# Kernel tuning notes

Hardware: AMD Instinct MI355X
Metric: run time of the kernel (lower is better)

## Reference

```python
import jax, jax.numpy as jnp
import numpy as np

A_BITS = 3
W_BITS = 3

def setup_inputs() -> dict:
    key = jax.random.key(0)
    k1, k2 = jax.random.split(key)
    # activations: small nonnegative ints (will be clipped to [0, 2^A_bits-1])
    x = jax.random.randint(k1, (32, 256, 56, 56), 0, 2 ** A_BITS, dtype=jnp.int32)
    # weights: torch.randint(0, 2**W_bits - 1, ...) -> values in [0, 6]
    weight = jax.random.randint(k2, (256, 256, 3, 3), 0, 2 ** W_BITS - 1).astype(jnp.float32)
    return {"x": x, "weight": weight}

def reference(x, weight):
    # quantize: clip activations to [0, 2^A_bits - 1]; truncate weight to int
    xq = jnp.clip(x.astype(jnp.int32), 0, 2 ** A_BITS - 1).astype(jnp.float32)
    wq = weight.astype(jnp.int32).astype(jnp.float32)  # OIHW, nonneg small ints
    # direct conv2d, stride 1, no padding (VALID). Small ints -> exact in fp32.
    out = jax.lax.conv_general_dilated(
        xq, wq,
        window_strides=(1, 1),
        padding="VALID",
        dimension_numbers=("NCHW", "OIHW", "NCHW"),
    )
    return out  # [32, 256, 54, 54]
```

## Files before the change

### kernel.cpp

```cpp
#include <hip/hip_runtime.h>
#include <stdint.h>

typedef int i32x4 __attribute__((ext_vector_type(4)));

#define N_IMG 32
#define C_IN 256
#define H_IN 56
#define W_IN 56
#define K_OUT 256
#define H_OUT 54
#define W_OUT 54
#define HW_OUT 2916
#define M_PIX 93312
#define CHW_OUT 746496

#define XT_BYTES ((size_t)N_IMG * H_IN * W_IN * C_IN)
#define WT_BYTES ((size_t)9 * K_OUT * C_IN)

__global__ __launch_bounds__(256) void xform_x(const int* __restrict__ x,
                                               unsigned char* __restrict__ xt) {
    const int bid = blockIdx.x;
    const int n = bid / H_IN;
    const int h = bid % H_IN;
    const int c = threadIdx.x;
    const int* src = x + ((size_t)((n * C_IN + c) * H_IN + h)) * W_IN;
    unsigned char* dst = xt + ((size_t)(n * H_IN + h) * W_IN) * C_IN + c;
    #pragma unroll
    for (int w0 = 0; w0 < W_IN; w0 += 4) {
        int4 v = *(const int4*)(src + w0);
        int a[4] = {v.x, v.y, v.z, v.w};
        #pragma unroll
        for (int j = 0; j < 4; ++j) {
            int q = a[j] < 0 ? 0 : (a[j] > 7 ? 7 : a[j]);
            dst[(size_t)(w0 + j) * C_IN] = (unsigned char)q;
        }
    }
}

__global__ __launch_bounds__(256) void xform_w(const float* __restrict__ w,
                                               unsigned char* __restrict__ wt) {
    const int k = blockIdx.x;
    const int c = threadIdx.x;
    const float* src = w + ((size_t)k * C_IN + c) * 9;
    #pragma unroll
    for (int rs = 0; rs < 9; ++rs) {
        int iv = (int)src[rs];
        wt[((size_t)rs * K_OUT + k) * C_IN + c] = (unsigned char)iv;
    }
}

__device__ __forceinline__ void gload_lds16(const void* g, void* l) {
    __builtin_amdgcn_global_load_lds(
        (const __attribute__((address_space(1))) uint32_t*)g,
        (__attribute__((address_space(3))) uint32_t*)l,
        16, 0, 0);
}

__global__ __launch_bounds__(256) void conv_mfma(const unsigned char* __restrict__ xt,
                                                 const unsigned char* __restrict__ wt,
                                                 float* __restrict__ out) {
    __shared__ unsigned char As[128 * 128];
    __shared__ unsigned char Bs[128 * 128];

    const int t   = threadIdx.x;
    const int l   = t & 63;
    const int wid = t >> 6;
    const int wr  = wid >> 1;
    const int wc  = wid & 1;
    const int mb  = blockIdx.x >> 1;
    const int nb  = blockIdx.x & 1;

    const int cs = (((l & 7) ^ (l >> 3)) << 4);

    int abase[4], bbase[4];
    #pragma unroll
    for (int i = 0; i < 4; ++i) {
        const int row = i * 32 + wid * 8 + (l >> 3);
        const int m   = mb * 128 + row;
        const int n   = m / HW_OUT;
        const int rem = m - n * HW_OUT;
        const int ho  = rem / W_OUT;
        const int wo  = rem - ho * W_OUT;
        abase[i] = (((n * H_IN + ho) * W_IN + wo) << 8) + cs;
        bbase[i] = ((nb * 128 + row) << 8) + cs;
    }

    i32x4 acc[4][4];
    #pragma unroll
    for (int i = 0; i < 4; ++i)
        #pragma unroll
        for (int j = 0; j < 4; ++j)
            acc[i][j] = (i32x4){0, 0, 0, 0};

    const char* xb = (const char*)xt;
    const char* wb = (const char*)wt;
    char* Ab = (char*)As;
    char* Bb = (char*)Bs;

    const int lrow = l & 15;
    const int lk   = (l >> 4) << 4;

    for (int ks = 0; ks < 18; ++ks) {
        const int rs  = ks >> 1;
        const int c0b = (ks & 1) << 7;
        const int r   = rs / 3;
        const int s   = rs - r * 3;
        const int astep = ((r * W_IN + s) << 8) + c0b;
        const int bstep = rs * (K_OUT * C_IN) + c0b;

        __syncthreads();
        #pragma unroll
        for (int i = 0; i < 4; ++i) {
            gload_lds16(xb + abase[i] + astep, Ab + i * 4096 + wid * 1024);
            gload_lds16(wb + bbase[i] + bstep, Bb + i * 4096 + wid * 1024);
        }
        __syncthreads();

        i32x4 af[4][2], bfv[4][2];
        #pragma unroll
        for (int f = 0; f < 4; ++f) {
            const int arow = wr * 64 + f * 16 + lrow;
            const int brow = wc * 64 + f * 16 + lrow;
            const int asw = (arow & 7) << 4;
            const int bsw = (brow & 7) << 4;
            #pragma unroll
            for (int kk = 0; kk < 2; ++kk) {
                const int chb = (kk << 6) + lk;
                af[f][kk]  = *(const i32x4*)(Ab + (arow << 7) + (chb ^ asw));
                bfv[f][kk] = *(const i32x4*)(Bb + (brow << 7) + (chb ^ bsw));
            }
        }
        #pragma unroll
        for (int mf = 0; mf < 4; ++mf)
            #pragma unroll
            for (int nf = 0; nf < 4; ++nf)
                #pragma unroll
                for (int kk = 0; kk < 2; ++kk)
                    acc[mf][nf] = __builtin_amdgcn_mfma_i32_16x16x64_i8(
                        af[mf][kk], bfv[nf][kk], acc[mf][nf], 0, 0, 0);
    }

    const int c16    = l & 15;
    const int p4     = (l >> 4) << 2;
    const int chbase = nb * 128 + wc * 64 + c16;
    #pragma unroll
    for (int mf = 0; mf < 4; ++mf) {
        #pragma unroll
        for (int j = 0; j < 4; ++j) {
            const int m   = mb * 128 + wr * 64 + mf * 16 + p4 + j;
            const int n   = m / HW_OUT;
            const int rem = m - n * HW_OUT;
            float* obase = out + (size_t)n * CHW_OUT + rem;
            #pragma unroll
            for (int nf = 0; nf < 4; ++nf)
                obase[(size_t)(chbase + nf * 16) * HW_OUT] = (float)acc[mf][nf][j];
        }
    }
}

__global__ __launch_bounds__(256) void conv_naive(const int* __restrict__ x,
                                                  const float* __restrict__ w,
                                                  float* __restrict__ out) {
    int idx = blockIdx.x * 256 + threadIdx.x;
    if (idx >= N_IMG * K_OUT * HW_OUT) return;
    const int wo = idx % W_OUT;
    int tmp = idx / W_OUT;
    const int ho = tmp % H_OUT; tmp /= H_OUT;
    const int k = tmp % K_OUT;
    const int n = tmp / K_OUT;
    float acc = 0.f;
    for (int c = 0; c < C_IN; ++c) {
        const int* xp = x + ((size_t)((n * C_IN + c) * H_IN + ho)) * W_IN + wo;
        const float* wp = w + ((size_t)(k * C_IN + c)) * 9;
        #pragma unroll
        for (int r = 0; r < 3; ++r)
            #pragma unroll
            for (int s = 0; s < 3; ++s) {
                int xv = xp[r * W_IN + s];
                xv = xv < 0 ? 0 : (xv > 7 ? 7 : xv);
                acc += (float)xv * (float)(int)wp[r * 3 + s];
            }
    }
    out[idx] = acc;
}

extern "C" void kernel_launch(void* const* d_in, const int* in_sizes, int n_in,
                              void* d_out, int out_size, void* d_ws, size_t ws_size,
                              hipStream_t stream) {
    const int*   x = (const int*)d_in[0];
    const float* w = (const float*)d_in[1];
    float* out = (float*)d_out;

    const size_t need = XT_BYTES + WT_BYTES;
    if (ws_size >= need) {
        unsigned char* xt = (unsigned char*)d_ws;
        unsigned char* wt = (unsigned char*)((char*)d_ws + XT_BYTES);
        hipLaunchKernelGGL(xform_x, dim3(N_IMG * H_IN), dim3(256), 0, stream, x, xt);
        hipLaunchKernelGGL(xform_w, dim3(K_OUT), dim3(256), 0, stream, w, wt);
        hipLaunchKernelGGL(conv_mfma, dim3((M_PIX / 128) * 2), dim3(256), 0, stream, xt, wt, out);
    } else {
        const int total = N_IMG * K_OUT * HW_OUT;
        hipLaunchKernelGGL(conv_naive, dim3((total + 255) / 256), dim3(256), 0, stream, x, w, out);
    }
}
```

Before: 102.6 us.

## Triple-buffer conv MFMA main loop with 512-thread 128x256 tiles

Reworks the int8 MFMA implicit-GEMM conv kernel. Each block now covers all 256 output channels with 8 waves (128x256 tile) instead of two blocks of 128x128, and a 3-stage LDS ring with global_load_lds prefetch two k-steps ahead is interleaved with split MFMA phases, using explicit barriers, waitcnt and setprio. The aim is to overlap global loads with MFMA work and halve the redundant activation loads. It uses 144KB of LDS per block and hand-tuned synchronisation, which risks low occupancy and subtle ordering bugs.

```diff
diff --git a/kernel.cpp b/kernel.cpp
--- a/kernel.cpp
+++ b/kernel.cpp
@@ -56,34 +56,131 @@
         16, 0, 0);
 }
 
-__global__ __launch_bounds__(256) void conv_mfma(const unsigned char* __restrict__ xt,
-                                                 const unsigned char* __restrict__ wt,
-                                                 float* __restrict__ out) {
-    __shared__ unsigned char As[128 * 128];
-    __shared__ unsigned char Bs[128 * 128];
-
-    const int t   = threadIdx.x;
-    const int l   = t & 63;
-    const int wid = t >> 6;
-    const int wr  = wid >> 1;
-    const int wc  = wid & 1;
-    const int mb  = blockIdx.x >> 1;
-    const int nb  = blockIdx.x & 1;
-
-    const int cs = (((l & 7) ^ (l >> 3)) << 4);
-
-    int abase[4], bbase[4];
-    #pragma unroll
-    for (int i = 0; i < 4; ++i) {
-        const int row = i * 32 + wid * 8 + (l >> 3);
-        const int m   = mb * 128 + row;
+__device__ __forceinline__ unsigned lds_off(const void* p) {
+    return (unsigned)(unsigned long long)(__attribute__((address_space(3))) const char*)p;
+}
+
+#define DSREAD(dst, addr) \
+    asm volatile("ds_read_b128 %0, %1" : "=v"(dst) : "v"(addr))
+#define WAIT_LGKM0 asm volatile("s_waitcnt lgkmcnt(0)" ::: "memory")
+
+template <bool PRE, int VM>
+__device__ __forceinline__ void kstep(int T, unsigned CA, unsigned CB,
+                                      unsigned char* PA, unsigned char* PB,
+                                      const char* xb, const char* wb,
+                                      const int* abase, const int* bbase,
+                                      const unsigned (&aoff)[4][2],
+                                      const unsigned (&boff)[4][2],
+                                      int tb16, i32x4 (&acc)[4][4]) {
+    int astp = 0, bstp = 0;
+    if constexpr (PRE) {
+        const int tp = T + 2;
+        const int rp = tp >> 1, cp = (tp & 1) << 7;
+        const int rr = rp / 3, ss = rp - rr * 3;
+        astp = ((rr * W_IN + ss) << 8) + cp;
+        bstp = rp * (K_OUT * C_IN) + cp;
+    }
+    i32x4 af[4][2], bf[4][2];
+    #pragma unroll
+    for (int mf = 0; mf < 4; ++mf)
+        #pragma unroll
+        for (int kk = 0; kk < 2; ++kk)
+            DSREAD(af[mf][kk], CA + aoff[mf][kk]);
+    #pragma unroll
+    for (int nf = 0; nf < 2; ++nf)
+        #pragma unroll
+        for (int kk = 0; kk < 2; ++kk)
+            DSREAD(bf[nf][kk], CB + boff[nf][kk]);
+    if constexpr (PRE) {
+        gload_lds16(xb + abase[0] + astp, PA + tb16);
+        gload_lds16(xb + abase[1] + astp, PA + 8192 + tb16);
+        gload_lds16(wb + bbase[0] + bstp, PB + tb16);
+    }
+    __builtin_amdgcn_s_barrier();
+    WAIT_LGKM0;
+    __builtin_amdgcn_sched_barrier(0);
+    __builtin_amdgcn_s_setprio(1);
+    #pragma unroll
+    for (int mf = 0; mf < 4; ++mf)
+        #pragma unroll
+        for (int nf = 0; nf < 2; ++nf)
+            #pragma unroll
+            for (int kk = 0; kk < 2; ++kk)
+                acc[mf][nf] = __builtin_amdgcn_mfma_i32_16x16x64_i8(
+                    af[mf][kk], bf[nf][kk], acc[mf][nf], 0, 0, 0);
+    __builtin_amdgcn_s_setprio(0);
+    __builtin_amdgcn_s_barrier();
+    #pragma unroll
+    for (int nf = 2; nf < 4; ++nf)
+        #pragma unroll
+        for (int kk = 0; kk < 2; ++kk)
+            DSREAD(bf[nf][kk], CB + boff[nf][kk]);
+    if constexpr (PRE) {
+        gload_lds16(wb + bbase[1] + bstp, PB + 8192 + tb16);
+        gload_lds16(wb + bbase[2] + bstp, PB + 16384 + tb16);
+        gload_lds16(wb + bbase[3] + bstp, PB + 24576 + tb16);
+    }
+    __builtin_amdgcn_s_barrier();
+    WAIT_LGKM0;
+    __builtin_amdgcn_sched_barrier(0);
+    __builtin_amdgcn_s_setprio(1);
+    #pragma unroll
+    for (int mf = 0; mf < 4; ++mf)
+        #pragma unroll
+        for (int nf = 2; nf < 4; ++nf)
+            #pragma unroll
+            for (int kk = 0; kk < 2; ++kk)
+                acc[mf][nf] = __builtin_amdgcn_mfma_i32_16x16x64_i8(
+                    af[mf][kk], bf[nf][kk], acc[mf][nf], 0, 0, 0);
+    __builtin_amdgcn_s_setprio(0);
+    if constexpr (VM == 6) asm volatile("s_waitcnt vmcnt(6)" ::: "memory");
+    else if constexpr (VM == 0) asm volatile("s_waitcnt vmcnt(0)" ::: "memory");
+    if constexpr (VM >= 0) __builtin_amdgcn_s_barrier();
+}
+
+__global__ __launch_bounds__(512, 2) void conv_mfma(const unsigned char* __restrict__ xt,
+                                                    const unsigned char* __restrict__ wt,
+                                                    float* __restrict__ out) {
+    __shared__ __align__(16) unsigned char As[3 * 16384];
+    __shared__ __align__(16) unsigned char Bs[3 * 32768];
+
+    const int t512 = threadIdx.x;
+    const int l    = t512 & 63;
+    const int wid  = t512 >> 6;
+    const int wr   = wid >> 2;
+    const int wc   = wid & 3;
+    const int mb   = blockIdx.x;
+
+    const int srow = t512 >> 3;
+    const int cs   = (((t512 & 7) ^ (srow & 7)) << 4);
+    const int tb16 = t512 * 16;
+
+    int abase[2], bbase[4];
+    #pragma unroll
+    for (int i = 0; i < 2; ++i) {
+        const int m   = mb * 128 + i * 64 + srow;
         const int n   = m / HW_OUT;
         const int rem = m - n * HW_OUT;
         const int ho  = rem / W_OUT;
         const int wo  = rem - ho * W_OUT;
         abase[i] = (((n * H_IN + ho) * W_IN + wo) << 8) + cs;
-        bbase[i] = ((nb * 128 + row) << 8) + cs;
-    }
+    }
+    #pragma unroll
+    for (int j = 0; j < 4; ++j)
+        bbase[j] = ((j * 64 + srow) << 8) + cs;
+
+    const int lrow = l & 15;
+    const int lkb  = (l >> 4) << 4;
+    const unsigned swz = (unsigned)((lrow & 7) << 4);
+    unsigned aoff[4][2], boff[4][2];
+    #pragma unroll
+    for (int f = 0; f < 4; ++f)
+        #pragma unroll
+        for (int kk = 0; kk < 2; ++kk) {
+            const unsigned kb = (unsigned)(((kk << 6) + lkb)) ^ swz;
+            aoff[f][kk] = (unsigned)(((wr * 64 + f * 16 + lrow) << 7)) + kb;
+            boff[f][kk] = (unsigned)(((wc * 64 + f * 16 + lrow) << 7)) + kb;
+        }
 
     i32x4 acc[4][4];
     #pragma unroll
@@ -94,55 +191,44 @@
 
     const char* xb = (const char*)xt;
     const char* wb = (const char*)wt;
-    char* Ab = (char*)As;
-    char* Bb = (char*)Bs;
-
-    const int lrow = l & 15;
-    const int lk   = (l >> 4) << 4;
-
-    for (int ks = 0; ks < 18; ++ks) {
-        const int rs  = ks >> 1;
-        const int c0b = (ks & 1) << 7;
-        const int r   = rs / 3;
-        const int s   = rs - r * 3;
-        const int astep = ((r * W_IN + s) << 8) + c0b;
-        const int bstep = rs * (K_OUT * C_IN) + c0b;
-
-        __syncthreads();
-        #pragma unroll
-        for (int i = 0; i < 4; ++i) {
-            gload_lds16(xb + abase[i] + astep, Ab + i * 4096 + wid * 1024);
-            gload_lds16(wb + bbase[i] + bstep, Bb + i * 4096 + wid * 1024);
-        }
-        __syncthreads();
-
-        i32x4 af[4][2], bfv[4][2];
-        #pragma unroll
-        for (int f = 0; f < 4; ++f) {
-            const int arow = wr * 64 + f * 16 + lrow;
-            const int brow = wc * 64 + f * 16 + lrow;
-            const int asw = (arow & 7) << 4;
-            const int bsw = (brow & 7) << 4;
-            #pragma unroll
-            for (int kk = 0; kk < 2; ++kk) {
-                const int chb = (kk << 6) + lk;
-                af[f][kk]  = *(const i32x4*)(Ab + (arow << 7) + (chb ^ asw));
-                bfv[f][kk] = *(const i32x4*)(Bb + (brow << 7) + (chb ^ bsw));
-            }
-        }
-        #pragma unroll
-        for (int mf = 0; mf < 4; ++mf)
-            #pragma unroll
-            for (int nf = 0; nf < 4; ++nf)
-                #pragma unroll
-                for (int kk = 0; kk < 2; ++kk)
-                    acc[mf][nf] = __builtin_amdgcn_mfma_i32_16x16x64_i8(
-                        af[mf][kk], bfv[nf][kk], acc[mf][nf], 0, 0, 0);
-    }
-
-    const int c16    = l & 15;
-    const int p4     = (l >> 4) << 2;
-    const int chbase = nb * 128 + wc * 64 + c16;
+    unsigned char* A0p = As;
+    unsigned char* A1p = As + 16384;
+    unsigned char* A2p = As + 32768;
+    unsigned char* B0p = Bs;
+    unsigned char* B1p = Bs + 32768;
+    unsigned char* B2p = Bs + 65536;
+    const unsigned a0 = lds_off(A0p), a1 = a0 + 16384, a2 = a0 + 32768;
+    const unsigned b0 = lds_off(B0p), b1 = b0 + 32768, b2 = b0 + 65536;
+
+    #define STAGE6(T, PA, PB) do {                                         \
+        const int rp_ = (T) >> 1, cp_ = ((T) & 1) << 7;                    \
+        const int rr_ = rp_ / 3, ss_ = rp_ - rr_ * 3;                      \
+        const int ast_ = ((rr_ * W_IN + ss_) << 8) + cp_;                  \
+        const int bst_ = rp_ * (K_OUT * C_IN) + cp_;                       \
+        gload_lds16(xb + abase[0] + ast_, (PA) + tb16);                    \
+        gload_lds16(xb + abase[1] + ast_, (PA) + 8192 + tb16);             \
+        gload_lds16(wb + bbase[0] + bst_, (PB) + tb16);                    \
+        gload_lds16(wb + bbase[1] + bst_, (PB) + 8192 + tb16);             \
+        gload_lds16(wb + bbase[2] + bst_, (PB) + 16384 + tb16);            \
+        gload_lds16(wb + bbase[3] + bst_, (PB) + 24576 + tb16);            \
+    } while (0)
+
+    STAGE6(0, A0p, B0p);
+    STAGE6(1, A1p, B1p);
+    asm volatile("s_waitcnt vmcnt(6)" ::: "memory");
+    __builtin_amdgcn_s_barrier();
+
+    for (int tb = 0; tb < 15; tb += 3) {
+        kstep<true, 6>(tb + 0, a0, b0, A2p, B2p, xb, wb, abase, bbase, aoff, boff, tb16, acc);
+        kstep<true, 6>(tb + 1, a1, b1, A0p, B0p, xb, wb, abase, bbase, aoff, boff, tb16, acc);
+        kstep<true, 6>(tb + 2, a2, b2, A1p, B1p, xb, wb, abase, bbase, aoff, boff, tb16, acc);
+    }
+    kstep<true, 6>(15, a0, b0, A2p, B2p, xb, wb, abase, bbase, aoff, boff, tb16, acc);
+    kstep<false, 0>(16, a1, b1, A2p, B2p, xb, wb, abase, bbase, aoff, boff, tb16, acc);
+    kstep<false, -1>(17, a2, b2, A2p, B2p, xb, wb, abase, bbase, aoff, boff, tb16, acc);
+
+    const int c16 = l & 15;
+    const int p4  = (l >> 4) << 2;
     #pragma unroll
     for (int mf = 0; mf < 4; ++mf) {
         #pragma unroll
@@ -152,10 +238,13 @@
             const int rem = m - n * HW_OUT;
             float* obase = out + (size_t)n * CHW_OUT + rem;
             #pragma unroll
-            for (int nf = 0; nf < 4; ++nf)
-                obase[(size_t)(chbase + nf * 16) * HW_OUT] = (float)acc[mf][nf][j];
+            for (int nf = 0; nf < 4; ++nf) {
+                const int ch = wc * 64 + nf * 16 + c16;
+                obase[(size_t)ch * HW_OUT] = (float)acc[mf][nf][j];
+            }
         }
     }
+    #undef STAGE6
 }
 
 __global__ __launch_bounds__(256) void conv_naive(const int* __restrict__ x,
@@ -197,7 +286,7 @@
         unsigned char* wt = (unsigned char*)((char*)d_ws + XT_BYTES);
         hipLaunchKernelGGL(xform_x, dim3(N_IMG * H_IN), dim3(256), 0, stream, x, xt);
         hipLaunchKernelGGL(xform_w, dim3(K_OUT), dim3(256), 0, stream, w, wt);
-        hipLaunchKernelGGL(conv_mfma, dim3((M_PIX / 128) * 2), dim3(256), 0, stream, xt, wt, out);
+        hipLaunchKernelGGL(conv_mfma, dim3(M_PIX / 128), dim3(512), 0, stream, xt, wt, out);
     } else {
         const int total = N_IMG * K_OUT * HW_OUT;
         hipLaunchKernelGGL(conv_naive, dim3((total + 255) / 256), dim3(256), 0, stream, x, w, out);
```

Result: slower. 138.5 us (+35.0%).

## Double-buffer LDS in 192x256 tile conv with merged transform kernel and vector stores

Applied to the files above, without the earlier changes.

Changes the int8 MFMA conv tile from 128x128 to 192x256 with 512 threads per block, so each block covers all output channels and A tiles are loaded once. LDS is double-buffered, and the next stage's global-to-LDS loads are issued between the two halves of the LDS fragment reads, leaving one barrier per K step. It also uses inline ds_read, setprio and sched barriers, writes outputs as float4 vectors, and merges the two transform kernels into one launch. The cost is 112KB of LDS and many more accumulator registers, which may limit occupancy.

```diff
diff --git a/kernel.cpp b/kernel.cpp
--- a/kernel.cpp
+++ b/kernel.cpp
@@ -2,6 +2,7 @@
 #include <stdint.h>
 
 typedef int i32x4 __attribute__((ext_vector_type(4)));
+typedef float f32x4 __attribute__((ext_vector_type(4)));
 
 #define N_IMG 32
 #define C_IN 256
@@ -14,38 +15,46 @@
 #define M_PIX 93312
 #define CHW_OUT 746496
 
+#define BM 192
+#define NSTEP 18
+
 #define XT_BYTES ((size_t)N_IMG * H_IN * W_IN * C_IN)
 #define WT_BYTES ((size_t)9 * K_OUT * C_IN)
 
-__global__ __launch_bounds__(256) void xform_x(const int* __restrict__ x,
-                                               unsigned char* __restrict__ xt) {
+#define A_OFF1 24576
+#define B_OFF0 49152
+#define B_STRIDE 32768
+
+__global__ __launch_bounds__(256) void xform(const int* __restrict__ x,
+                                             const float* __restrict__ w,
+                                             unsigned char* __restrict__ xt,
+                                             unsigned char* __restrict__ wt) {
     const int bid = blockIdx.x;
-    const int n = bid / H_IN;
-    const int h = bid % H_IN;
-    const int c = threadIdx.x;
-    const int* src = x + ((size_t)((n * C_IN + c) * H_IN + h)) * W_IN;
-    unsigned char* dst = xt + ((size_t)(n * H_IN + h) * W_IN) * C_IN + c;
-    #pragma unroll
-    for (int w0 = 0; w0 < W_IN; w0 += 4) {
-        int4 v = *(const int4*)(src + w0);
-        int a[4] = {v.x, v.y, v.z, v.w};
-        #pragma unroll
-        for (int j = 0; j < 4; ++j) {
-            int q = a[j] < 0 ? 0 : (a[j] > 7 ? 7 : a[j]);
-            dst[(size_t)(w0 + j) * C_IN] = (unsigned char)q;
+    if (bid < N_IMG * H_IN) {
+        const int n = bid / H_IN;
+        const int h = bid % H_IN;
+        const int c = threadIdx.x;
+        const int* src = x + ((size_t)((n * C_IN + c) * H_IN + h)) * W_IN;
+        unsigned char* dst = xt + ((size_t)(n * H_IN + h) * W_IN) * C_IN + c;
+        #pragma unroll
+        for (int w0 = 0; w0 < W_IN; w0 += 4) {
+            int4 v = *(const int4*)(src + w0);
+            int a[4] = {v.x, v.y, v.z, v.w};
+            #pragma unroll
+            for (int j = 0; j < 4; ++j) {
+                int q = a[j] < 0 ? 0 : (a[j] > 7 ? 7 : a[j]);
+                dst[(size_t)(w0 + j) * C_IN] = (unsigned char)q;
+            }
         }
-    }
-}
-
-__global__ __launch_bounds__(256) void xform_w(const float* __restrict__ w,
-                                               unsigned char* __restrict__ wt) {
-    const int k = blockIdx.x;
-    const int c = threadIdx.x;
-    const float* src = w + ((size_t)k * C_IN + c) * 9;
-    #pragma unroll
-    for (int rs = 0; rs < 9; ++rs) {
-        int iv = (int)src[rs];
-        wt[((size_t)rs * K_OUT + k) * C_IN + c] = (unsigned char)iv;
+    } else {
+        const int k = bid - N_IMG * H_IN;
+        const int c = threadIdx.x;
+        const float* src = w + ((size_t)k * C_IN + c) * 9;
+        #pragma unroll
+        for (int rs = 0; rs < 9; ++rs) {
+            int iv = (int)src[rs];
+            wt[((size_t)rs * K_OUT + k) * C_IN + c] = (unsigned char)iv;
+        }
     }
 }
 
@@ -56,106 +65,145 @@
         16, 0, 0);
 }
 
-__global__ __launch_bounds__(256) void conv_mfma(const unsigned char* __restrict__ xt,
-                                                 const unsigned char* __restrict__ wt,
-                                                 float* __restrict__ out) {
-    __shared__ unsigned char As[128 * 128];
-    __shared__ unsigned char Bs[128 * 128];
-
-    const int t   = threadIdx.x;
-    const int l   = t & 63;
-    const int wid = t >> 6;
-    const int wr  = wid >> 1;
-    const int wc  = wid & 1;
-    const int mb  = blockIdx.x >> 1;
-    const int nb  = blockIdx.x & 1;
-
-    const int cs = (((l & 7) ^ (l >> 3)) << 4);
-
-    int abase[4], bbase[4];
-    #pragma unroll
-    for (int i = 0; i < 4; ++i) {
-        const int row = i * 32 + wid * 8 + (l >> 3);
-        const int m   = mb * 128 + row;
+__device__ __forceinline__ unsigned lds_off(const void* p) {
+    return (unsigned)(unsigned long long)(__attribute__((address_space(3))) const char*)p;
+}
+
+#define DSREAD(dst, addr) \
+    asm volatile("ds_read_b128 %0, %1" : "=v"(dst) : "v"(addr))
+
+__global__ __launch_bounds__(512, 2) void conv_mfma(const unsigned char* __restrict__ xt,
+                                                    const unsigned char* __restrict__ wt,
+                                                    float* __restrict__ out) {
+    __shared__ __align__(16) unsigned char lds[114688];
+
+    const int t512 = threadIdx.x;
+    const int l    = t512 & 63;
+    const int wid  = t512 >> 6;
+    const int wr   = wid >> 2;
+    const int wc   = wid & 3;
+    const int mb   = blockIdx.x;
+
+    const int srow = t512 >> 3;
+    const int cs   = (((t512 & 7) ^ (srow & 7)) << 4);
+    const int tb16 = t512 * 16;
+
+    int abase[3], bbase[4];
+    #pragma unroll
+    for (int i = 0; i < 3; ++i) {
+        const int m   = mb * BM + i * 64 + srow;
         const int n   = m / HW_OUT;
         const int rem = m - n * HW_OUT;
         const int ho  = rem / W_OUT;
         const int wo  = rem - ho * W_OUT;
         abase[i] = (((n * H_IN + ho) * W_IN + wo) << 8) + cs;
-        bbase[i] = ((nb * 128 + row) << 8) + cs;
-    }
-
-    i32x4 acc[4][4];
-    #pragma unroll
-    for (int i = 0; i < 4; ++i)
+    }
+    #pragma unroll
+    for (int j = 0; j < 4; ++j)
+        bbase[j] = ((j * 64 + srow) << 8) + cs;
+
+    const int lrow = l & 15;
+    const int lk   = (l >> 4) << 4;
+    const unsigned swz = (unsigned)((lrow & 7) << 4);
+    const unsigned colk[2] = { ((unsigned)lk) ^ swz, ((unsigned)(64 + lk)) ^ swz };
+    unsigned arow128[6], brow128[4];
+    #pragma unroll
+    for (int mf = 0; mf < 6; ++mf) arow128[mf] = (unsigned)((wr * 96 + mf * 16 + lrow) << 7);
+    #pragma unroll
+    for (int nf = 0; nf < 4; ++nf) brow128[nf] = (unsigned)((wc * 64 + nf * 16 + lrow) << 7);
+
+    i32x4 acc[6][4];
+    #pragma unroll
+    for (int i = 0; i < 6; ++i)
         #pragma unroll
         for (int j = 0; j < 4; ++j)
             acc[i][j] = (i32x4){0, 0, 0, 0};
 
     const char* xb = (const char*)xt;
     const char* wb = (const char*)wt;
-    char* Ab = (char*)As;
-    char* Bb = (char*)Bs;
-
-    const int lrow = l & 15;
-    const int lk   = (l >> 4) << 4;
-
-    for (int ks = 0; ks < 18; ++ks) {
-        const int rs  = ks >> 1;
-        const int c0b = (ks & 1) << 7;
-        const int r   = rs / 3;
-        const int s   = rs - r * 3;
-        const int astep = ((r * W_IN + s) << 8) + c0b;
-        const int bstep = rs * (K_OUT * C_IN) + c0b;
-
-        __syncthreads();
-        #pragma unroll
-        for (int i = 0; i < 4; ++i) {
-            gload_lds16(xb + abase[i] + astep, Ab + i * 4096 + wid * 1024);
-            gload_lds16(wb + bbase[i] + bstep, Bb + i * 4096 + wid * 1024);
+    const unsigned ldsb = lds_off(lds);
+
+    #define STAGE(T, SEL) do {                                              \
+        const int rs_ = (T) >> 1, ch_ = ((T) & 1) << 7;                     \
+        const int r_ = rs_ / 3, s_ = rs_ - r_ * 3;                          \
+        const int ast_ = ((r_ * W_IN + s_) << 8) + ch_;                     \
+        const int bst_ = rs_ * (K_OUT * C_IN) + ch_;                        \
+        unsigned char* pa_ = lds + (SEL) * A_OFF1 + tb16;                   \
+        unsigned char* pb_ = lds + B_OFF0 + (SEL) * B_STRIDE + tb16;        \
+        gload_lds16(xb + abase[0] + ast_, pa_);                             \
+        gload_lds16(xb + abase[1] + ast_, pa_ + 8192);                      \
+        gload_lds16(xb + abase[2] + ast_, pa_ + 16384);                     \
+        gload_lds16(wb + bbase[0] + bst_, pb_);                             \
+        gload_lds16(wb + bbase[1] + bst_, pb_ + 8192);                      \
+        gload_lds16(wb + bbase[2] + bst_, pb_ + 16384);                     \
+        gload_lds16(wb + bbase[3] + bst_, pb_ + 24576);                     \
+    } while (0)
+
+    #define KBODY(CUR, DO_STAGE, TN) do {                                   \
+        const unsigned aB = ldsb + (CUR) * A_OFF1;                          \
+        const unsigned bB = ldsb + B_OFF0 + (CUR) * B_STRIDE;               \
+        i32x4 a0[6], b0[4], a1[6], b1[4];                                   \
+        _Pragma("unroll")                                                   \
+        for (int mf = 0; mf < 6; ++mf) DSREAD(a0[mf], aB + arow128[mf] + colk[0]); \
+        _Pragma("unroll")                                                   \
+        for (int nf = 0; nf < 4; ++nf) DSREAD(b0[nf], bB + brow128[nf] + colk[0]); \
+        if (DO_STAGE) STAGE(TN, ((TN) & 1));                                \
+        _Pragma("unroll")                                                   \
+        for (int mf = 0; mf < 6; ++mf) DSREAD(a1[mf], aB + arow128[mf] + colk[1]); \
+        _Pragma("unroll")                                                   \
+        for (int nf = 0; nf < 4; ++nf) DSREAD(b1[nf], bB + brow128[nf] + colk[1]); \
+        asm volatile("s_waitcnt lgkmcnt(10)" ::: "memory");                 \
+        __builtin_amdgcn_sched_barrier(0);                                  \
+        __builtin_amdgcn_s_setprio(1);                                      \
+        _Pragma("unroll")                                                   \
+        for (int mf = 0; mf < 6; ++mf)                                      \
+            _Pragma("unroll")                                               \
+            for (int nf = 0; nf < 4; ++nf)                                  \
+                acc[mf][nf] = __builtin_amdgcn_mfma_i32_16x16x64_i8(        \
+                    a0[mf], b0[nf], acc[mf][nf], 0, 0, 0);                  \
+        __builtin_amdgcn_s_setprio(0);                                      \
+        asm volatile("s_waitcnt lgkmcnt(0)" ::: "memory");                  \
+        __builtin_amdgcn_sched_barrier(0);                                  \
+        __builtin_amdgcn_s_setprio(1);                                      \
+        _Pragma("unroll")                                                   \
+        for (int mf = 0; mf < 6; ++mf)                                      \
+            _Pragma("unroll")                                               \
+            for (int nf = 0; nf < 4; ++nf)                                  \
+                acc[mf][nf] = __builtin_amdgcn_mfma_i32_16x16x64_i8(        \
+                    a1[mf], b1[nf], acc[mf][nf], 0, 0, 0);                  \
+        __builtin_amdgcn_s_setprio(0);                                      \
+    } while (0)
+
+    STAGE(0, 0);
+    asm volatile("s_waitcnt vmcnt(0)" ::: "memory");
+    __builtin_amdgcn_s_barrier();
+
+    for (int t = 0; t < NSTEP - 1; ++t) {
+        KBODY((t & 1), 1, (t + 1));
+        asm volatile("s_waitcnt vmcnt(0)" ::: "memory");
+        __builtin_amdgcn_s_barrier();
+    }
+    KBODY(((NSTEP - 1) & 1), 0, 0);
+
+    const int c16 = l & 15;
+    const int p4  = (l >> 4) << 2;
+    #pragma unroll
+    for (int mf = 0; mf < 6; ++mf) {
+        const int m   = mb * BM + wr * 96 + mf * 16 + p4;
+        const int n   = m / HW_OUT;
+        const int rem = m - n * HW_OUT;
+        float* ob = out + (size_t)n * CHW_OUT + rem;
+        #pragma unroll
+        for (int nf = 0; nf < 4; ++nf) {
+            const int ch = wc * 64 + nf * 16 + c16;
+            f32x4 v;
+            #pragma unroll
+            for (int j = 0; j < 4; ++j) v[j] = (float)acc[mf][nf][j];
+            *(f32x4*)(ob + (size_t)ch * HW_OUT) = v;
         }
-        __syncthreads();
-
-        i32x4 af[4][2], bfv[4][2];
-        #pragma unroll
-        for (int f = 0; f < 4; ++f) {
-            const int arow = wr * 64 + f * 16 + lrow;
-            const int brow = wc * 64 + f * 16 + lrow;
-            const int asw = (arow & 7) << 4;
-            const int bsw = (brow & 7) << 4;
-            #pragma unroll
-            for (int kk = 0; kk < 2; ++kk) {
-                const int chb = (kk << 6) + lk;
-                af[f][kk]  = *(const i32x4*)(Ab + (arow << 7) + (chb ^ asw));
-                bfv[f][kk] = *(const i32x4*)(Bb + (brow << 7) + (chb ^ bsw));
-            }
-        }
-        #pragma unroll
-        for (int mf = 0; mf < 4; ++mf)
-            #pragma unroll
-            for (int nf = 0; nf < 4; ++nf)
-                #pragma unroll
-                for (int kk = 0; kk < 2; ++kk)
-                    acc[mf][nf] = __builtin_amdgcn_mfma_i32_16x16x64_i8(
-                        af[mf][kk], bfv[nf][kk], acc[mf][nf], 0, 0, 0);
-    }
-
-    const int c16    = l & 15;
-    const int p4     = (l >> 4) << 2;
-    const int chbase = nb * 128 + wc * 64 + c16;
-    #pragma unroll
-    for (int mf = 0; mf < 4; ++mf) {
-        #pragma unroll
-        for (int j = 0; j < 4; ++j) {
-            const int m   = mb * 128 + wr * 64 + mf * 16 + p4 + j;
-            const int n   = m / HW_OUT;
-            const int rem = m - n * HW_OUT;
-            float* obase = out + (size_t)n * CHW_OUT + rem;
-            #pragma unroll
-            for (int nf = 0; nf < 4; ++nf)
-                obase[(size_t)(chbase + nf * 16) * HW_OUT] = (float)acc[mf][nf][j];
-        }
-    }
+    }
+    #undef KBODY
+    #undef STAGE
 }
 
 __global__ __launch_bounds__(256) void conv_naive(const int* __restrict__ x,
@@ -195,9 +243,10 @@
     if (ws_size >= need) {
         unsigned char* xt = (unsigned char*)d_ws;
         unsigned char* wt = (unsigned char*)((char*)d_ws + XT_BYTES);
-        hipLaunchKernelGGL(xform_x, dim3(N_IMG * H_IN), dim3(256), 0, stream, x, xt);
-        hipLaunchKernelGGL(xform_w, dim3(K_OUT), dim3(256), 0, stream, w, wt);
-        hipLaunchKernelGGL(conv_mfma, dim3((M_PIX / 128) * 2), dim3(256), 0, stream, xt, wt, out);
+        hipLaunchKernelGGL(xform, dim3(N_IMG * H_IN + K_OUT), dim3(256), 0, stream,
+                           x, w, xt, wt);
+        hipLaunchKernelGGL(conv_mfma, dim3(M_PIX / BM), dim3(512), 0, stream,
+                           xt, wt, out);
     } else {
         const int total = N_IMG * K_OUT * HW_OUT;
         hipLaunchKernelGGL(conv_naive, dim3((total + 255) / 256), dim3(256), 0, stream, x, w, out);
```

Measured after the change: 88.99 us. -13.3%, faster.
